# Kernel tuning notes

Measured on AMD Instinct MI355X. Metric: run time of the kernel, lower is better.

## Reference

```python
import jax, jax.numpy as jnp
import numpy as np

B, K_SLOTS, P = 4096, 8, 768
SLOT = P // 3          # 256, slot feature dim
HID = 256              # pres/up hidden width
NC, NP = 512, 512
LN_EPS = 1e-5


def _layernorm(x, g, b):
    m = jnp.mean(x, axis=-1, keepdims=True)
    v = jnp.var(x, axis=-1, keepdims=True)
    return (x - m) * jax.lax.rsqrt(v + LN_EPS) * g + b


def _mlp2(x, W1, b1, g, bt, W2, b2):
    # Linear -> LayerNorm -> ReLU -> Linear (torchvision ops.MLP with hidden=[256, out])
    h = jax.nn.relu(_layernorm(x @ W1 + b1, g, bt))
    return h @ W2 + b2


def setup_inputs() -> dict:
    key = jax.random.key(0)
    ks = jax.random.split(key, 24)
    rn = lambda k, shp, s=1.0: jax.random.normal(k, shp, dtype=jnp.float32) * s
    d = {
        "inst_embed": rn(ks[0], (B, P)),
        "slots": rn(ks[1], (B, K_SLOTS, SLOT)),
        # fc / fp: single Linear(p, p)
        "Wfc": rn(ks[2], (P, P), 1.0 / np.sqrt(P)),
        "bfc": jnp.zeros((P,), jnp.float32),
        "Wfp": rn(ks[3], (P, P), 1.0 / np.sqrt(P)),
        "bfp": jnp.zeros((P,), jnp.float32),
        # memory codebooks (plain randn per the original)
        "Kc": rn(ks[4], (NC, P)),
        "Vc": rn(ks[5], (NC, P)),
        "Kp": rn(ks[6], (NP, P)),
        "Vp": rn(ks[7], (NP, P)),
        # pres MLP: Linear(4p/3,256)+LN+ReLU, Linear(256,p/3)
        "pres_W1": rn(ks[8], (SLOT + P, HID), 1.0 / np.sqrt(SLOT + P)),
        "pres_b1": jnp.zeros((HID,), jnp.float32),
        "pres_g": jnp.ones((HID,), jnp.float32),
        "pres_bt": jnp.zeros((HID,), jnp.float32),
        "pres_W2": rn(ks[9], (HID, SLOT), 1.0 / np.sqrt(HID)),
        "pres_b2": jnp.zeros((SLOT,), jnp.float32),
        # up MLP: same shapes
        "up_W1": rn(ks[10], (SLOT + P, HID), 1.0 / np.sqrt(SLOT + P)),
        "up_b1": jnp.zeros((HID,), jnp.float32),
        "up_g": jnp.ones((HID,), jnp.float32),
        "up_bt": jnp.zeros((HID,), jnp.float32),
        "up_W2": rn(ks[11], (HID, SLOT), 1.0 / np.sqrt(HID)),
        "up_b2": jnp.zeros((SLOT,), jnp.float32),
    }
    return d


def reference(inst_embed, slots, Wfc, bfc, Wfp, bfp, Kc, Vc, Kp, Vp,
              pres_W1, pres_b1, pres_g, pres_bt, pres_W2, pres_b2,
              up_W1, up_b1, up_g, up_bt, up_W2, up_b2):
    scale = jnp.float32(np.sqrt(P))
    # selection: soft attention over the two codebooks
    Qc = inst_embed @ Wfc + bfc                     # [B, P]
    Qp = inst_embed @ Wfp + bfp                     # [B, P]
    c = jax.nn.softmax(jnp.einsum('bi,ci->bc', Qc, Kc) / scale, axis=-1) @ Vc  # [B, P]
    p = jax.nn.softmax(jnp.einsum('bi,pi->bp', Qp, Kp) / scale, axis=-1) @ Vp  # [B, P]
    # update: vectorized over the K slot loop of the original
    cb = jnp.broadcast_to(c[:, None, :], (B, K_SLOTS, P))
    pb = jnp.broadcast_to(p[:, None, :], (B, K_SLOTS, P))
    hc = jnp.concatenate([slots, cb], axis=-1)      # [B, K, SLOT+P]
    hp = jnp.concatenate([slots, pb], axis=-1)      # [B, K, SLOT+P]
    gate_pres = _mlp2(hc, pres_W1, pres_b1, pres_g, pres_bt, pres_W2, pres_b2)
    gate_up = _mlp2(hp, up_W1, up_b1, up_g, up_bt, up_W2, up_b2)
    return slots + gate_pres * gate_up              # [B, K, SLOT]
```

## Files before the change

kernel.cpp:

```cpp
#include <hip/hip_runtime.h>
#include <stdint.h>

#define BB    4096
#define KS    8
#define PP    768
#define SLOT  256
#define HID   256
#define NC    512
#define BKROWS (BB*KS)
typedef unsigned short u16;
typedef short bf16x8 __attribute__((ext_vector_type(8)));
typedef float f32x4  __attribute__((ext_vector_type(4)));

__device__ __forceinline__ u16 f2bf(float x) {
  union { float f; uint32_t u; } v; v.f = x;
  return (u16)((v.u + 0x7FFFu + ((v.u >> 16) & 1u)) >> 16);
}

__device__ __forceinline__ u16 f2h(float x) {
  union { _Float16 h; u16 u; } cv; cv.h = (_Float16)x; return cv.u;
}
__device__ __forceinline__ float h2f(u16 x) {
  union { u16 u; _Float16 h; } cv; cv.u = x; return (float)cv.h;
}

__device__ __forceinline__ void gload_lds16(u16* ldst, const u16* gsrc) {
  __builtin_amdgcn_global_load_lds(
      (const __attribute__((address_space(1))) void*)gsrc,
      (__attribute__((address_space(3))) void*)ldst, 16, 0, 0);
}

template<int EPI>
__device__ __forceinline__ void gemm_core64(
    const u16* __restrict__ A, int lda,
    const u16* __restrict__ B, int ldb,
    const float* __restrict__ bias,
    void* __restrict__ out, int ldo, int K,
    int blockRow, int blockCol, u16* lsA, u16* lsB)
{
  const int tid  = threadIdx.x;
  const int w    = tid >> 6;
  const int lane = tid & 63;
  const int wm   = w >> 1, wn = w & 1;
  const int rl   = lane >> 4, cl = lane & 15;

  f32x4 acc[2][4];
  const f32x4 zero = {0.f, 0.f, 0.f, 0.f};
#pragma unroll
  for (int i = 0; i < 2; ++i)
#pragma unroll
    for (int j = 0; j < 4; ++j) acc[i][j] = zero;

  const u16* Ablk = A + (size_t)blockRow * lda;
  const u16* Bblk = B + (size_t)blockCol * ldb;

  for (int k0 = 0; k0 < K; k0 += 64) {
#pragma unroll
    for (int i = 0; i < 2; ++i) {
      int seg   = i * 4 + w;
      int off16 = seg * 64 + lane;
      int row   = off16 >> 3;
      int chunk = (off16 & 7) ^ (row & 7);
      gload_lds16(lsA + seg * 512, Ablk + (size_t)row * lda + k0 + chunk * 8);
    }
#pragma unroll
    for (int i = 0; i < 4; ++i) {
      int seg   = i * 4 + w;
      int off16 = seg * 64 + lane;
      int row   = off16 >> 3;
      int chunk = (off16 & 7) ^ (row & 7);
      gload_lds16(lsB + seg * 512, Bblk + (size_t)row * ldb + k0 + chunk * 8);
    }
    __syncthreads();

#pragma unroll
    for (int ks = 0; ks < 2; ++ks) {
      bf16x8 aF[2], bF[4];
#pragma unroll
      for (int f = 0; f < 2; ++f) {
        int r  = wm * 32 + f * 16 + cl;
        int ca = ((ks * 4 + rl) ^ (r & 7)) * 8;
        aF[f] = *(const bf16x8*)(lsA + r * 64 + ca);
      }
#pragma unroll
      for (int f = 0; f < 4; ++f) {
        int rn = wn * 64 + f * 16 + cl;
        int cb = ((ks * 4 + rl) ^ (rn & 7)) * 8;
        bF[f] = *(const bf16x8*)(lsB + rn * 64 + cb);
      }
#pragma unroll
      for (int fm = 0; fm < 2; ++fm)
#pragma unroll
        for (int fn = 0; fn < 4; ++fn)
          acc[fm][fn] = __builtin_amdgcn_mfma_f32_16x16x32_bf16(
              aF[fm], bF[fn], acc[fm][fn], 0, 0, 0);
    }
    __syncthreads();
  }

#pragma unroll
  for (int fm = 0; fm < 2; ++fm) {
#pragma unroll
    for (int fn = 0; fn < 4; ++fn) {
      f32x4 v = acc[fm][fn];
#pragma unroll
      for (int r = 0; r < 4; ++r) {
        int grow = blockRow + wm * 32 + fm * 16 + rl * 4 + r;
        int gcol = blockCol + wn * 64 + fn * 16 + cl;
        float x = v[r];
        if constexpr (EPI == 2) {
          ((u16*)out)[(size_t)grow * ldo + gcol] = f2bf(x);
        } else if constexpr (EPI == 3) {
          x += bias[gcol];
          ((float*)out)[(size_t)grow * ldo + gcol] = x;
        } else if constexpr (EPI == 5) {
          x += bias[gcol];
          ((u16*)out)[(size_t)grow * ldo + gcol] = f2h(x);
        }
      }
    }
  }
}

template<int EPI>
__device__ __forceinline__ void gemm_core6464(
    const u16* __restrict__ A, int lda,
    const u16* __restrict__ B, int ldb,
    const float* __restrict__ bias,
    void* __restrict__ out, int ldo, int K,
    int blockRow, int blockCol, u16* lsA, u16* lsB)
{
  const int tid  = threadIdx.x;
  const int w    = tid >> 6;
  const int lane = tid & 63;
  const int wm   = w >> 1, wn = w & 1;
  const int rl   = lane >> 4, cl = lane & 15;

  f32x4 acc[2][2];
  const f32x4 zero = {0.f, 0.f, 0.f, 0.f};
#pragma unroll
  for (int i = 0; i < 2; ++i)
#pragma unroll
    for (int j = 0; j < 2; ++j) acc[i][j] = zero;

  const u16* Ablk = A + (size_t)blockRow * lda;
  const u16* Bblk = B + (size_t)blockCol * ldb;

  for (int k0 = 0; k0 < K; k0 += 64) {
#pragma unroll
    for (int i = 0; i < 2; ++i) {
      int seg   = i * 4 + w;
      int off16 = seg * 64 + lane;
      int row   = off16 >> 3;
      int chunk = (off16 & 7) ^ (row & 7);
      gload_lds16(lsA + seg * 512, Ablk + (size_t)row * lda + k0 + chunk * 8);
    }
#pragma unroll
    for (int i = 0; i < 2; ++i) {
      int seg   = i * 4 + w;
      int off16 = seg * 64 + lane;
      int row   = off16 >> 3;
      int chunk = (off16 & 7) ^ (row & 7);
      gload_lds16(lsB + seg * 512, Bblk + (size_t)row * ldb + k0 + chunk * 8);
    }
    __syncthreads();

#pragma unroll
    for (int ks = 0; ks < 2; ++ks) {
      bf16x8 aF[2], bF[2];
#pragma unroll
      for (int f = 0; f < 2; ++f) {
        int r  = wm * 32 + f * 16 + cl;
        int ca = ((ks * 4 + rl) ^ (r & 7)) * 8;
        aF[f] = *(const bf16x8*)(lsA + r * 64 + ca);
        int rn = wn * 32 + f * 16 + cl;
        int cb = ((ks * 4 + rl) ^ (rn & 7)) * 8;
        bF[f] = *(const bf16x8*)(lsB + rn * 64 + cb);
      }
#pragma unroll
      for (int fm = 0; fm < 2; ++fm)
#pragma unroll
        for (int fn = 0; fn < 2; ++fn)
          acc[fm][fn] = __builtin_amdgcn_mfma_f32_16x16x32_bf16(
              aF[fm], bF[fn], acc[fm][fn], 0, 0, 0);
    }
    __syncthreads();
  }

#pragma unroll
  for (int fm = 0; fm < 2; ++fm) {
#pragma unroll
    for (int fn = 0; fn < 2; ++fn) {
      f32x4 v = acc[fm][fn];
#pragma unroll
      for (int r = 0; r < 4; ++r) {
        int grow = blockRow + wm * 32 + fm * 16 + rl * 4 + r;
        int gcol = blockCol + wn * 32 + fn * 16 + cl;
        float x = v[r];
        if constexpr (EPI == 2) {
          ((u16*)out)[(size_t)grow * ldo + gcol] = f2bf(x);
        } else if constexpr (EPI == 3) {
          x += bias[gcol];
          ((float*)out)[(size_t)grow * ldo + gcol] = x;
        } else if constexpr (EPI == 5) {
          x += bias[gcol];
          ((u16*)out)[(size_t)grow * ldo + gcol] = f2h(x);
        }
      }
    }
  }
}

__device__ __forceinline__ void cvt_seg(const float* __restrict__ in,
                                        u16* __restrict__ outp, int b, int n4) {
  int i = b * 256 + threadIdx.x;
  if (i < n4) {
    float4 v = ((const float4*)in)[i];
    ushort4 o;
    o.x = f2bf(v.x); o.y = f2bf(v.y); o.z = f2bf(v.z); o.w = f2bf(v.w);
    ((ushort4*)outp)[i] = o;
  }
}

__device__ __forceinline__ void pack_seg(const float* __restrict__ s0,
                                         const float* __restrict__ s1,
                                         u16* __restrict__ dst, int b) {
  int br = b >> 4, ng = b & 15;
  const float* src = br ? s1 : s0;
  int w = threadIdx.x >> 6, lane = threadIdx.x & 63;
  int rl = lane >> 4, cl = lane & 15;
#pragma unroll
  for (int s = 0; s < 2; ++s) {
    int step = w * 2 + s;
    union { u16 u[8]; uint4 q; } o;
#pragma unroll
    for (int j = 0; j < 8; ++j)
      o.u[j] = f2bf(src[(size_t)(step * 32 + rl * 8 + j) * 256 + ng * 16 + cl]);
    *(uint4*)(dst + (size_t)(((br * 16 + ng) * 8 + step) * 64 + lane) * 8) = o.q;
  }
}

__global__ __launch_bounds__(256) void prep_all(
    const float* __restrict__ inst, const float* __restrict__ Kc,
    const float* __restrict__ Kp, const float* __restrict__ Wfc,
    const float* __restrict__ Wfp, const float* __restrict__ Vc,
    const float* __restrict__ Vp, const float* __restrict__ pW1,
    const float* __restrict__ uW1, const float* __restrict__ pW2,
    const float* __restrict__ uW2, const float* __restrict__ bfc,
    const float* __restrict__ bfp,
    u16* instb, u16* Kcb, u16* Kpb, u16* Wfcb, u16* Wfpb, u16* Vcb, u16* Vpb,
    u16* W1Tp, u16* W1Tu, u16* W1pk, u16* W2pk, float* sb)
{
  __shared__ float tile[32][33];
  int b = blockIdx.x;
  if (b < 3072)      { cvt_seg(inst, instb, b,        786432); return; }
  else if (b < 3456) { cvt_seg(Kc,   Kcb,   b - 3072,  98304); return; }
  else if (b < 3840) { cvt_seg(Kp,   Kpb,   b - 3456,  98304); return; }
  else if (b < 4416) { cvt_seg(Wfc,  Wfcb,  b - 3840, 147456); return; }
  else if (b < 4992) { cvt_seg(Wfp,  Wfpb,  b - 4416, 147456); return; }
  else if (b < 5376) { cvt_seg(Vc,   Vcb,   b - 4992,  98304); return; }
  else if (b < 5760) { cvt_seg(Vp,   Vpb,   b - 5376,  98304); return; }
  else if (b < 6272) {
    int bb = b - 5760;
    const float* in = (bb < 256) ? pW1 : uW1;
    u16* outp = (bb < 256) ? W1Tp : W1Tu;
    bb &= 255;
    int tc = (bb & 7) * 32, tr = (bb >> 3) * 32;
    int lx = threadIdx.x & 31, ly = threadIdx.x >> 5;
#pragma unroll
    for (int i = 0; i < 32; i += 8)
      tile[ly + i][lx] = in[(size_t)(tr + ly + i) * 256 + tc + lx];
    __syncthreads();
#pragma unroll
    for (int i = 0; i < 32; i += 8)
      outp[(size_t)(tc + ly + i) * 1024 + tr + lx] = f2bf(tile[lx][ly + i]);
    return;
  }
  else if (b < 6304) { pack_seg(pW1, uW1, W1pk, b - 6272); return; }
  else if (b < 6336) { pack_seg(pW2, uW2, W2pk, b - 6304); return; }
  else {
    int w = threadIdx.x >> 6, lane = threadIdx.x & 63;
    int row = (b - 6336) * 4 + w;
    int br = row >> 9, n = row & 511;
    const float* Kr = (br ? Kp : Kc) + (size_t)n * PP;
    const float* bf = br ? bfp : bfc;
    float s = 0.f;
#pragma unroll
    for (int j = 0; j < 12; ++j) s += Kr[lane + j * 64] * bf[lane + j * 64];
#pragma unroll
    for (int o = 32; o; o >>= 1) s += __shfl_xor(s, o);
    if (!lane) sb[row] = s;
  }
}

__global__ __launch_bounds__(256) void gemm_mixed(
    const u16* Kcb, const u16* Kpb, const u16* Wfcb, const u16* Wfpb,
    u16* KWc, u16* KWp,
    const u16* W1Tp, const u16* W1Tu, const u16* Vcb, const u16* Vpb,
    u16* VW1p, u16* VW1u)
{
  __shared__ u16 lsA[64 * 64];
  __shared__ u16 lsB[128 * 64];
  int b = blockIdx.x;
  if (b < 96) {
    int z = b / 48, r = b % 48;
    gemm_core64<2>(z ? Kpb : Kcb, PP, z ? Wfpb : Wfcb, PP, nullptr,
                   z ? KWp : KWc, PP, PP, (r & 7) * 64, (r >> 3) * 128, lsA, lsB);
  } else {
    int c = b - 96, z = c / 16, r = c % 16;
    gemm_core64<2>((z ? W1Tu : W1Tp) + 256, 1024, z ? Vpb : Vcb, PP, nullptr,
                   z ? VW1u : VW1p, NC, PP, (r & 3) * 64, (r >> 2) * 128, lsA, lsB);
  }
}

__global__ __launch_bounds__(256) void gemm_scores(
    const u16* instb, const u16* KW, const float* sb, u16* scH)
{
  __shared__ u16 lsA[64 * 64];
  __shared__ u16 lsB[64 * 64];
  gemm_core6464<5>(instb, PP, KW, PP, sb, scH, 1024, PP,
                   blockIdx.x * 64, blockIdx.y * 64, lsA, lsB);
}

__global__ __launch_bounds__(256) void gemm_t(
    const u16* Pb, const u16* VW1p, const u16* VW1u,
    const float* pb1, const float* ub1, float* t0, float* t1)
{
  __shared__ u16 lsA[64 * 64];
  __shared__ u16 lsB[64 * 64];
  int z = blockIdx.z;
  gemm_core6464<3>(Pb + (size_t)z * BB * NC, NC, z ? VW1u : VW1p, NC,
                   z ? ub1 : pb1, z ? t1 : t0, SLOT, NC,
                   blockIdx.x * 64, blockIdx.y * 64, lsA, lsB);
}

__global__ __launch_bounds__(256) void softmax_rows(const u16* __restrict__ scH,
                                                    u16* __restrict__ Pp) {
  int w = threadIdx.x >> 6, lane = threadIdx.x & 63;
  int row = blockIdx.x * 4 + w;
  int i = row >> 1, b = row & 1;
  const u16* src = scH + (size_t)i * 1024 + b * 512 + lane * 8;
  uint4 q = *(const uint4*)src;
  const u16* hp = (const u16*)&q;
  float vv[8];
#pragma unroll
  for (int j = 0; j < 8; ++j) vv[j] = h2f(hp[j]);
  float m = vv[0];
#pragma unroll
  for (int j = 1; j < 8; ++j) m = fmaxf(m, vv[j]);
#pragma unroll
  for (int o = 32; o; o >>= 1) m = fmaxf(m, __shfl_xor(m, o));
  const float alpha = 0.03608439182435161f;
  float e[8], s = 0.f;
#pragma unroll
  for (int j = 0; j < 8; ++j) { e[j] = __expf((vv[j] - m) * alpha); s += e[j]; }
#pragma unroll
  for (int o = 32; o; o >>= 1) s += __shfl_xor(s, o);
  float inv = 1.f / s;
  union { u16 u[8]; uint4 q; } ou;
#pragma unroll
  for (int j = 0; j < 8; ++j) ou.u[j] = f2bf(e[j] * inv);
  *(uint4*)(Pp + ((size_t)b * BB + i) * 512 + lane * 8) = ou.q;
}

__global__ __launch_bounds__(512, 4) void fused_update(
    const float* __restrict__ slots,
    const float* __restrict__ t0, const float* __restrict__ t1,
    const u16* __restrict__ W1pk, const u16* __restrict__ W2pk,
    const float* __restrict__ pg, const float* __restrict__ pbt,
    const float* __restrict__ ug, const float* __restrict__ ubt,
    const float* __restrict__ pb2, const float* __restrict__ ub2,
    float* __restrict__ outp)
{
  __shared__ u16 lsH[2][32 * 256];
  __shared__ float lstat[2][32][16];
  __shared__ float lfin[2][32][2];

  const int tid = threadIdx.x, w = tid >> 6, lane = tid & 63;
  const int rl = lane >> 4, cl = lane & 15;
  const int blockRow = blockIdx.x * 32;

  u16* lsA = lsH[0];

#pragma unroll
  for (int it = 0; it < 4; ++it) {
    int L = it * 512 + tid;
    int row = L >> 6, qc = L & 63;
    float4 v = *(const float4*)(slots + (size_t)(blockRow + row) * 256 + qc * 4);
    ushort4 b; b.x = f2bf(v.x); b.y = f2bf(v.y); b.z = f2bf(v.z); b.w = f2bf(v.w);
    int chunk = qc >> 1, half = qc & 1;
    *(ushort4*)(lsA + row * 256 + (((chunk ^ (row & 7)) << 3) + half * 4)) = b;
  }
  __syncthreads();

  f32x4 acc[2][4];
  const f32x4 zero = {0.f, 0.f, 0.f, 0.f};
#pragma unroll
  for (int i = 0; i < 2; ++i)
#pragma unroll
    for (int j = 0; j < 4; ++j) acc[i][j] = zero;

#define MF(A, B, C) C = __builtin_amdgcn_mfma_f32_16x16x32_bf16(A, B, C, 0, 0, 0);

  {
    bf16x8 pb[3][2], ub[3][2];
#define FR1(NG, S) (*(const bf16x8*)(W1pk + (size_t)(((NG) * 8 + (S)) * 64 + lane) * 8))
#define LDW1(SL, S) { pb[SL][0] = FR1(w * 2, S);      pb[SL][1] = FR1(w * 2 + 1, S);  \
                      ub[SL][0] = FR1(16 + w * 2, S); ub[SL][1] = FR1(17 + w * 2, S); \
                      asm volatile("" ::: "memory"); }
    LDW1(0, 0) LDW1(1, 1) LDW1(2, 2)
#pragma unroll
    for (int s = 0; s < 8; ++s) {
      const int sl = s % 3;
      bf16x8 a0 = *(const bf16x8*)(lsA + cl * 256 + (((s * 4 + rl) ^ (cl & 7)) << 3));
      bf16x8 a1 = *(const bf16x8*)(lsA + (16 + cl) * 256 + (((s * 4 + rl) ^ (cl & 7)) << 3));
      MF(a0, pb[sl][0], acc[0][0]) MF(a1, pb[sl][0], acc[1][0])
      MF(a0, pb[sl][1], acc[0][1]) MF(a1, pb[sl][1], acc[1][1])
      MF(a0, ub[sl][0], acc[0][2]) MF(a1, ub[sl][0], acc[1][2])
      MF(a0, ub[sl][1], acc[0][3]) MF(a1, ub[sl][1], acc[1][3])
      if (s < 5) LDW1(sl, s + 3)
    }
#undef LDW1
#undef FR1
  }

#pragma unroll
  for (int fm = 0; fm < 2; ++fm) {
    size_t trr = (size_t)(blockIdx.x * 4 + fm * 2 + (rl >> 1)) * 256;
#pragma unroll
    for (int fn = 0; fn < 2; ++fn) {
      int col = w * 32 + fn * 16 + cl;
      float tp = t0[trr + col], tu = t1[trr + col];
#pragma unroll
      for (int r = 0; r < 4; ++r) {
        acc[fm][fn][r]     += tp;
        acc[fm][2 + fn][r] += tu;
      }
    }
  }

#pragma unroll
  for (int fm = 0; fm < 2; ++fm)
#pragma unroll
    for (int br = 0; br < 2; ++br) {
      f32x4 s = acc[fm][br * 2] + acc[fm][br * 2 + 1];
      f32x4 q = acc[fm][br * 2] * acc[fm][br * 2] + acc[fm][br * 2 + 1] * acc[fm][br * 2 + 1];
#pragma unroll
      for (int o = 1; o < 16; o <<= 1) {
#pragma unroll
        for (int r = 0; r < 4; ++r) {
          s[r] += __shfl_xor(s[r], o);
          q[r] += __shfl_xor(q[r], o);
        }
      }
      if (cl == 0) {
#pragma unroll
        for (int r = 0; r < 4; ++r) {
          int row = fm * 16 + rl * 4 + r;
          lstat[br][row][w]     = s[r];
          lstat[br][row][8 + w] = q[r];
        }
      }
    }
  __syncthreads();

  if (tid < 64) {
    int fb = tid >> 5, row = tid & 31;
    f32x4 a = *(const f32x4*)&lstat[fb][row][0];
    f32x4 b = *(const f32x4*)&lstat[fb][row][4];
    f32x4 c = *(const f32x4*)&lstat[fb][row][8];
    f32x4 d = *(const f32x4*)&lstat[fb][row][12];
    float ss = a[0] + a[1] + a[2] + a[3] + b[0] + b[1] + b[2] + b[3];
    float qq = c[0] + c[1] + c[2] + c[3] + d[0] + d[1] + d[2] + d[3];
    float mu = ss * (1.f / 256.f);
    lfin[fb][row][0] = mu;
    lfin[fb][row][1] = rsqrtf(qq * (1.f / 256.f) - mu * mu + 1e-5f);
  }
  __syncthreads();

  {
    float gv[2][2], btv[2][2];
#pragma unroll
    for (int fn = 0; fn < 2; ++fn) {
      int col = w * 32 + fn * 16 + cl;
      gv[0][fn] = pg[col];  btv[0][fn] = pbt[col];
      gv[1][fn] = ug[col];  btv[1][fn] = ubt[col];
    }
#pragma unroll
    for (int fm = 0; fm < 2; ++fm) {
      float mean[2][4], rstd[2][4];
#pragma unroll
      for (int r = 0; r < 4; ++r) {
        int row = fm * 16 + rl * 4 + r;
        mean[0][r] = lfin[0][row][0]; rstd[0][r] = lfin[0][row][1];
        mean[1][r] = lfin[1][row][0]; rstd[1][r] = lfin[1][row][1];
      }
#pragma unroll
      for (int br = 0; br < 2; ++br)
#pragma unroll
        for (int fn = 0; fn < 2; ++fn) {
          int col = w * 32 + fn * 16 + cl;
#pragma unroll
          for (int r = 0; r < 4; ++r) {
            int row = fm * 16 + rl * 4 + r;
            float h = fmaxf((acc[fm][br * 2 + fn][r] - mean[br][r]) * rstd[br][r]
                            * gv[br][fn] + btv[br][fn], 0.f);
            lsH[br][row * 256 + (((col >> 3) ^ (row & 7)) << 3) + (col & 7)] = f2bf(h);
          }
        }
    }
  }
#pragma unroll
  for (int i = 0; i < 2; ++i)
#pragma unroll
    for (int j = 0; j < 4; ++j) acc[i][j] = zero;
  __syncthreads();

  const int brw = w >> 2, wc = w & 3;
  const u16* hsrc = lsH[brw];
  const float* b2src = brw ? ub2 : pb2;
  float b2v[4];
#pragma unroll
  for (int fn = 0; fn < 4; ++fn) b2v[fn] = b2src[wc * 64 + fn * 16 + cl];

  {
    bf16x8 bq[3][4];
#define FR2(NG, S) (*(const bf16x8*)(W2pk + (size_t)(((NG) * 8 + (S)) * 64 + lane) * 8))
#define LDW2(SL, S) { bq[SL][0] = FR2(brw * 16 + wc * 4,     S); \
                      bq[SL][1] = FR2(brw * 16 + wc * 4 + 1, S); \
                      bq[SL][2] = FR2(brw * 16 + wc * 4 + 2, S); \
                      bq[SL][3] = FR2(brw * 16 + wc * 4 + 3, S); \
                      asm volatile("" ::: "memory"); }
    LDW2(0, 0) LDW2(1, 1) LDW2(2, 2)
#pragma unroll
    for (int s = 0; s < 8; ++s) {
      const int sl = s % 3;
      bf16x8 a0 = *(const bf16x8*)(hsrc + cl * 256 + (((s * 4 + rl) ^ (cl & 7)) << 3));
      bf16x8 a1 = *(const bf16x8*)(hsrc + (16 + cl) * 256 + (((s * 4 + rl) ^ (cl & 7)) << 3));
      MF(a0, bq[sl][0], acc[0][0]) MF(a1, bq[sl][0], acc[1][0])
      MF(a0, bq[sl][1], acc[0][1]) MF(a1, bq[sl][1], acc[1][1])
      MF(a0, bq[sl][2], acc[0][2]) MF(a1, bq[sl][2], acc[1][2])
      MF(a0, bq[sl][3], acc[0][3]) MF(a1, bq[sl][3], acc[1][3])
      if (s < 5) LDW2(sl, s + 3)
    }
#undef LDW2
#undef FR2
  }
#undef MF
  __syncthreads();

  float* xbuf = (float*)&lsH[0][0];
  const int base = wc * 2048;
  if (brw == 0) {
#pragma unroll
    for (int fm = 0; fm < 2; ++fm)
#pragma unroll
      for (int fn = 0; fn < 4; ++fn)
#pragma unroll
        for (int r = 0; r < 4; ++r)
          xbuf[base + ((fm * 4 + fn) * 4 + r) * 64 + lane] = acc[fm][fn][r] + b2v[fn];
  }
  __syncthreads();

  if (brw == 1) {
#pragma unroll
    for (int fm = 0; fm < 2; ++fm)
#pragma unroll
      for (int fn = 0; fn < 4; ++fn)
#pragma unroll
        for (int r = 0; r < 4; ++r) {
          float gp = xbuf[base + ((fm * 4 + fn) * 4 + r) * 64 + lane];
          float gu = acc[fm][fn][r] + b2v[fn];
          int row = blockRow + fm * 16 + rl * 4 + r;
          int col = wc * 64 + fn * 16 + cl;
          size_t idx = (size_t)row * 256 + col;
          outp[idx] = slots[idx] + gp * gu;
        }
  }
}

extern "C" void kernel_launch(void* const* d_in, const int* in_sizes, int n_in,
                              void* d_out, int out_size, void* d_ws, size_t ws_size,
                              hipStream_t stream) {
  const float* inst  = (const float*)d_in[0];
  const float* slots = (const float*)d_in[1];
  const float* Wfc   = (const float*)d_in[2];
  const float* bfc   = (const float*)d_in[3];
  const float* Wfp   = (const float*)d_in[4];
  const float* bfp   = (const float*)d_in[5];
  const float* Kc    = (const float*)d_in[6];
  const float* Vc    = (const float*)d_in[7];
  const float* Kp    = (const float*)d_in[8];
  const float* Vp    = (const float*)d_in[9];
  const float* pW1   = (const float*)d_in[10];
  const float* pb1   = (const float*)d_in[11];
  const float* pg    = (const float*)d_in[12];
  const float* pbt   = (const float*)d_in[13];
  const float* pW2   = (const float*)d_in[14];
  const float* pb2   = (const float*)d_in[15];
  const float* uW1   = (const float*)d_in[16];
  const float* ub1   = (const float*)d_in[17];
  const float* ug    = (const float*)d_in[18];
  const float* ubt   = (const float*)d_in[19];
  const float* uW2   = (const float*)d_in[20];
  const float* ub2   = (const float*)d_in[21];
  float* out = (float*)d_out;
  char*  ws  = (char*)d_ws;

  const size_t OFF_INST  = 0;
  const size_t OFF_KC    = OFF_INST  + 6291456;
  const size_t OFF_KP    = OFF_KC    + 786432;
  const size_t OFF_WFCB  = OFF_KP    + 786432;
  const size_t OFF_WFPB  = OFF_WFCB  + 1179648;
  const size_t OFF_VCB   = OFF_WFPB  + 1179648;
  const size_t OFF_VPB   = OFF_VCB   + 786432;
  const size_t OFF_W1TP  = OFF_VPB   + 786432;
  const size_t OFF_W1TU  = OFF_W1TP  + 524288;
  const size_t OFF_W1PK  = OFF_W1TU  + 524288;
  const size_t OFF_W2PK  = OFF_W1PK  + 262144;
  const size_t OFF_KW    = OFF_W2PK  + 262144;
  const size_t OFF_VW1   = OFF_KW    + 1572864;
  const size_t OFF_SB    = OFF_VW1   + 524288;
  const size_t OFF_T     = OFF_SB    + 4096;
  const size_t OFF_SC    = OFF_T     + 8388608;
  const size_t OFF_P     = OFF_SC    + 8388608;

  u16*   instb = (u16*)(ws + OFF_INST);
  u16*   Kcb   = (u16*)(ws + OFF_KC);
  u16*   Kpb   = (u16*)(ws + OFF_KP);
  u16*   Wfcb  = (u16*)(ws + OFF_WFCB);
  u16*   Wfpb  = (u16*)(ws + OFF_WFPB);
  u16*   Vcb   = (u16*)(ws + OFF_VCB);
  u16*   Vpb   = (u16*)(ws + OFF_VPB);
  u16*   W1Tp  = (u16*)(ws + OFF_W1TP);
  u16*   W1Tu  = (u16*)(ws + OFF_W1TU);
  u16*   W1pk  = (u16*)(ws + OFF_W1PK);
  u16*   W2pk  = (u16*)(ws + OFF_W2PK);
  u16*   KWc   = (u16*)(ws + OFF_KW);
  u16*   KWp   = KWc + (size_t)NC * PP;
  u16*   VW1p  = (u16*)(ws + OFF_VW1);
  u16*   VW1u  = VW1p + (size_t)SLOT * NC;
  float* sb    = (float*)(ws + OFF_SB);
  float* t0    = (float*)(ws + OFF_T);
  float* t1    = t0 + (size_t)BB * SLOT;
  u16*   scH   = (u16*)(ws + OFF_SC);
  u16*   Pb    = (u16*)(ws + OFF_P);

  prep_all<<<dim3(6592), 256, 0, stream>>>(
      inst, Kc, Kp, Wfc, Wfp, Vc, Vp, pW1, uW1, pW2, uW2, bfc, bfp,
      instb, Kcb, Kpb, Wfcb, Wfpb, Vcb, Vpb, W1Tp, W1Tu, W1pk, W2pk, sb);

  gemm_mixed<<<dim3(128), 256, 0, stream>>>(
      Kcb, Kpb, Wfcb, Wfpb, KWc, KWp, W1Tp, W1Tu, Vcb, Vpb, VW1p, VW1u);

  gemm_scores<<<dim3(64, 16), 256, 0, stream>>>(instb, KWc, sb, scH);

  softmax_rows<<<dim3(2048), 256, 0, stream>>>(scH, Pb);

  gemm_t<<<dim3(64, 4, 2), 256, 0, stream>>>(Pb, VW1p, VW1u, pb1, ub1, t0, t1);

  fused_update<<<dim3(1024), 512, 0, stream>>>(
      slots, t0, t1, W1pk, W2pk, pg, pbt, ug, ubt, pb2, ub2, out);

  (void)in_sizes; (void)n_in; (void)out_size; (void)ws_size;
}
```

Baseline: 87.02 us.

## Fuse inst bf16 conversion into scores GEMM and retile precompute GEMMs

Removes the separate fp32->bf16 conversion pass over inst_embed from prep_all. The scores GEMM now loads fp32 inst rows directly, converts them in registers and writes swizzled bf16 into LDS, which avoids one write and one re-read of a 6 MB buffer. The mixed precompute GEMM switches to 64x64 tiles, doubling its block count to 256 for better CU coverage. The fused update kernel now issues the t0/t1 and W2 fragment loads earlier to overlap their latency with other work. In exchange, the scores kernel's A-tile load becomes a synchronous register path instead of an async LDS load, and each scores block repeats the conversion.

```diff
diff --git a/kernel.cpp b/kernel.cpp
--- a/kernel.cpp
+++ b/kernel.cpp
@@ -28,98 +28,6 @@
   __builtin_amdgcn_global_load_lds(
       (const __attribute__((address_space(1))) void*)gsrc,
       (__attribute__((address_space(3))) void*)ldst, 16, 0, 0);
-}
-
-template<int EPI>
-__device__ __forceinline__ void gemm_core64(
-    const u16* __restrict__ A, int lda,
-    const u16* __restrict__ B, int ldb,
-    const float* __restrict__ bias,
-    void* __restrict__ out, int ldo, int K,
-    int blockRow, int blockCol, u16* lsA, u16* lsB)
-{
-  const int tid  = threadIdx.x;
-  const int w    = tid >> 6;
-  const int lane = tid & 63;
-  const int wm   = w >> 1, wn = w & 1;
-  const int rl   = lane >> 4, cl = lane & 15;
-
-  f32x4 acc[2][4];
-  const f32x4 zero = {0.f, 0.f, 0.f, 0.f};
-#pragma unroll
-  for (int i = 0; i < 2; ++i)
-#pragma unroll
-    for (int j = 0; j < 4; ++j) acc[i][j] = zero;
-
-  const u16* Ablk = A + (size_t)blockRow * lda;
-  const u16* Bblk = B + (size_t)blockCol * ldb;
-
-  for (int k0 = 0; k0 < K; k0 += 64) {
-#pragma unroll
-    for (int i = 0; i < 2; ++i) {
-      int seg   = i * 4 + w;
-      int off16 = seg * 64 + lane;
-      int row   = off16 >> 3;
-      int chunk = (off16 & 7) ^ (row & 7);
-      gload_lds16(lsA + seg * 512, Ablk + (size_t)row * lda + k0 + chunk * 8);
-    }
-#pragma unroll
-    for (int i = 0; i < 4; ++i) {
-      int seg   = i * 4 + w;
-      int off16 = seg * 64 + lane;
-      int row   = off16 >> 3;
-      int chunk = (off16 & 7) ^ (row & 7);
-      gload_lds16(lsB + seg * 512, Bblk + (size_t)row * ldb + k0 + chunk * 8);
-    }
-    __syncthreads();
-
-#pragma unroll
-    for (int ks = 0; ks < 2; ++ks) {
-      bf16x8 aF[2], bF[4];
-#pragma unroll
-      for (int f = 0; f < 2; ++f) {
-        int r  = wm * 32 + f * 16 + cl;
-        int ca = ((ks * 4 + rl) ^ (r & 7)) * 8;
-        aF[f] = *(const bf16x8*)(lsA + r * 64 + ca);
-      }
-#pragma unroll
-      for (int f = 0; f < 4; ++f) {
-        int rn = wn * 64 + f * 16 + cl;
-        int cb = ((ks * 4 + rl) ^ (rn & 7)) * 8;
-        bF[f] = *(const bf16x8*)(lsB + rn * 64 + cb);
-      }
-#pragma unroll
-      for (int fm = 0; fm < 2; ++fm)
-#pragma unroll
-        for (int fn = 0; fn < 4; ++fn)
-          acc[fm][fn] = __builtin_amdgcn_mfma_f32_16x16x32_bf16(
-              aF[fm], bF[fn], acc[fm][fn], 0, 0, 0);
-    }
-    __syncthreads();
-  }
-
-#pragma unroll
-  for (int fm = 0; fm < 2; ++fm) {
-#pragma unroll
-    for (int fn = 0; fn < 4; ++fn) {
-      f32x4 v = acc[fm][fn];
-#pragma unroll
-      for (int r = 0; r < 4; ++r) {
-        int grow = blockRow + wm * 32 + fm * 16 + rl * 4 + r;
-        int gcol = blockCol + wn * 64 + fn * 16 + cl;
-        float x = v[r];
-        if constexpr (EPI == 2) {
-          ((u16*)out)[(size_t)grow * ldo + gcol] = f2bf(x);
-        } else if constexpr (EPI == 3) {
-          x += bias[gcol];
-          ((float*)out)[(size_t)grow * ldo + gcol] = x;
-        } else if constexpr (EPI == 5) {
-          x += bias[gcol];
-          ((u16*)out)[(size_t)grow * ldo + gcol] = f2h(x);
-        }
-      }
-    }
-  }
 }
 
 template<int EPI>
@@ -241,27 +149,25 @@
 }
 
 __global__ __launch_bounds__(256) void prep_all(
-    const float* __restrict__ inst, const float* __restrict__ Kc,
-    const float* __restrict__ Kp, const float* __restrict__ Wfc,
-    const float* __restrict__ Wfp, const float* __restrict__ Vc,
-    const float* __restrict__ Vp, const float* __restrict__ pW1,
-    const float* __restrict__ uW1, const float* __restrict__ pW2,
-    const float* __restrict__ uW2, const float* __restrict__ bfc,
-    const float* __restrict__ bfp,
-    u16* instb, u16* Kcb, u16* Kpb, u16* Wfcb, u16* Wfpb, u16* Vcb, u16* Vpb,
+    const float* __restrict__ Kc, const float* __restrict__ Kp,
+    const float* __restrict__ Wfc, const float* __restrict__ Wfp,
+    const float* __restrict__ Vc, const float* __restrict__ Vp,
+    const float* __restrict__ pW1, const float* __restrict__ uW1,
+    const float* __restrict__ pW2, const float* __restrict__ uW2,
+    const float* __restrict__ bfc, const float* __restrict__ bfp,
+    u16* Kcb, u16* Kpb, u16* Wfcb, u16* Wfpb, u16* Vcb, u16* Vpb,
     u16* W1Tp, u16* W1Tu, u16* W1pk, u16* W2pk, float* sb)
 {
   __shared__ float tile[32][33];
   int b = blockIdx.x;
-  if (b < 3072)      { cvt_seg(inst, instb, b,        786432); return; }
-  else if (b < 3456) { cvt_seg(Kc,   Kcb,   b - 3072,  98304); return; }
-  else if (b < 3840) { cvt_seg(Kp,   Kpb,   b - 3456,  98304); return; }
-  else if (b < 4416) { cvt_seg(Wfc,  Wfcb,  b - 3840, 147456); return; }
-  else if (b < 4992) { cvt_seg(Wfp,  Wfpb,  b - 4416, 147456); return; }
-  else if (b < 5376) { cvt_seg(Vc,   Vcb,   b - 4992,  98304); return; }
-  else if (b < 5760) { cvt_seg(Vp,   Vpb,   b - 5376,  98304); return; }
-  else if (b < 6272) {
-    int bb = b - 5760;
+  if (b < 384)       { cvt_seg(Kc,   Kcb,   b,         98304); return; }
+  else if (b < 768)  { cvt_seg(Kp,   Kpb,   b - 384,   98304); return; }
+  else if (b < 1344) { cvt_seg(Wfc,  Wfcb,  b - 768,  147456); return; }
+  else if (b < 1920) { cvt_seg(Wfp,  Wfpb,  b - 1344, 147456); return; }
+  else if (b < 2304) { cvt_seg(Vc,   Vcb,   b - 1920,  98304); return; }
+  else if (b < 2688) { cvt_seg(Vp,   Vpb,   b - 2304,  98304); return; }
+  else if (b < 3200) {
+    int bb = b - 2688;
     const float* in = (bb < 256) ? pW1 : uW1;
     u16* outp = (bb < 256) ? W1Tp : W1Tu;
     bb &= 255;
@@ -276,11 +182,11 @@
       outp[(size_t)(tc + ly + i) * 1024 + tr + lx] = f2bf(tile[lx][ly + i]);
     return;
   }
-  else if (b < 6304) { pack_seg(pW1, uW1, W1pk, b - 6272); return; }
-  else if (b < 6336) { pack_seg(pW2, uW2, W2pk, b - 6304); return; }
+  else if (b < 3232) { pack_seg(pW1, uW1, W1pk, b - 3200); return; }
+  else if (b < 3264) { pack_seg(pW2, uW2, W2pk, b - 3232); return; }
   else {
     int w = threadIdx.x >> 6, lane = threadIdx.x & 63;
-    int row = (b - 6336) * 4 + w;
+    int row = (b - 3264) * 4 + w;
     int br = row >> 9, n = row & 511;
     const float* Kr = (br ? Kp : Kc) + (size_t)n * PP;
     const float* bf = br ? bfp : bfc;
@@ -300,26 +206,103 @@
     u16* VW1p, u16* VW1u)
 {
   __shared__ u16 lsA[64 * 64];
-  __shared__ u16 lsB[128 * 64];
+  __shared__ u16 lsB[64 * 64];
   int b = blockIdx.x;
-  if (b < 96) {
-    int z = b / 48, r = b % 48;
-    gemm_core64<2>(z ? Kpb : Kcb, PP, z ? Wfpb : Wfcb, PP, nullptr,
-                   z ? KWp : KWc, PP, PP, (r & 7) * 64, (r >> 3) * 128, lsA, lsB);
+  if (b < 192) {
+    int z = b / 96, r = b % 96;
+    gemm_core6464<2>(z ? Kpb : Kcb, PP, z ? Wfpb : Wfcb, PP, nullptr,
+                     z ? KWp : KWc, PP, PP, (r & 7) * 64, (r >> 3) * 64, lsA, lsB);
   } else {
-    int c = b - 96, z = c / 16, r = c % 16;
-    gemm_core64<2>((z ? W1Tu : W1Tp) + 256, 1024, z ? Vpb : Vcb, PP, nullptr,
-                   z ? VW1u : VW1p, NC, PP, (r & 3) * 64, (r >> 2) * 128, lsA, lsB);
+    int c = b - 192, z = c / 32, r = c % 32;
+    gemm_core6464<2>((z ? W1Tu : W1Tp) + 256, 1024, z ? Vpb : Vcb, PP, nullptr,
+                     z ? VW1u : VW1p, NC, PP, (r & 3) * 64, (r >> 2) * 64, lsA, lsB);
   }
 }
 
 __global__ __launch_bounds__(256) void gemm_scores(
-    const u16* instb, const u16* KW, const float* sb, u16* scH)
+    const float* __restrict__ inst, const u16* __restrict__ KW,
+    const float* __restrict__ sb, u16* __restrict__ scH)
 {
   __shared__ u16 lsA[64 * 64];
   __shared__ u16 lsB[64 * 64];
-  gemm_core6464<5>(instb, PP, KW, PP, sb, scH, 1024, PP,
-                   blockIdx.x * 64, blockIdx.y * 64, lsA, lsB);
+  const int tid  = threadIdx.x;
+  const int w    = tid >> 6;
+  const int lane = tid & 63;
+  const int wm   = w >> 1, wn = w & 1;
+  const int rl   = lane >> 4, cl = lane & 15;
+  const int blockRow = blockIdx.x * 64;
+  const int blockCol = blockIdx.y * 64;
+
+  const int arow = tid >> 2;
+  const int kseg = (tid & 3) * 16;
+
+  f32x4 acc[2][2];
+  const f32x4 zero = {0.f, 0.f, 0.f, 0.f};
+#pragma unroll
+  for (int i = 0; i < 2; ++i)
+#pragma unroll
+    for (int j = 0; j < 2; ++j) acc[i][j] = zero;
+
+  const float* Asrc = inst + (size_t)(blockRow + arow) * PP + kseg;
+  const u16*   Bblk = KW + (size_t)blockCol * PP;
+
+  for (int k0 = 0; k0 < PP; k0 += 64) {
+    union { u16 u[8]; uint4 q; } c0, c1;
+#pragma unroll
+    for (int j = 0; j < 2; ++j) {
+      float4 v0 = *(const float4*)(Asrc + k0 + j * 8);
+      float4 v1 = *(const float4*)(Asrc + k0 + j * 8 + 4);
+      u16* dd = j ? c1.u : c0.u;
+      dd[0] = f2bf(v0.x); dd[1] = f2bf(v0.y); dd[2] = f2bf(v0.z); dd[3] = f2bf(v0.w);
+      dd[4] = f2bf(v1.x); dd[5] = f2bf(v1.y); dd[6] = f2bf(v1.z); dd[7] = f2bf(v1.w);
+    }
+    int cc = kseg >> 3;
+    *(uint4*)(lsA + arow * 64 + (((cc     ) ^ (arow & 7)) << 3)) = c0.q;
+    *(uint4*)(lsA + arow * 64 + (((cc + 1) ^ (arow & 7)) << 3)) = c1.q;
+#pragma unroll
+    for (int i = 0; i < 2; ++i) {
+      int seg   = i * 4 + w;
+      int off16 = seg * 64 + lane;
+      int row   = off16 >> 3;
+      int chunk = (off16 & 7) ^ (row & 7);
+      gload_lds16(lsB + seg * 512, Bblk + (size_t)row * PP + k0 + chunk * 8);
+    }
+    __syncthreads();
+
+#pragma unroll
+    for (int ks = 0; ks < 2; ++ks) {
+      bf16x8 aF[2], bF[2];
+#pragma unroll
+      for (int f = 0; f < 2; ++f) {
+        int r  = wm * 32 + f * 16 + cl;
+        int ca = ((ks * 4 + rl) ^ (r & 7)) * 8;
+        aF[f] = *(const bf16x8*)(lsA + r * 64 + ca);
+        int rn = wn * 32 + f * 16 + cl;
+        int cb = ((ks * 4 + rl) ^ (rn & 7)) * 8;
+        bF[f] = *(const bf16x8*)(lsB + rn * 64 + cb);
+      }
+#pragma unroll
+      for (int fm = 0; fm < 2; ++fm)
+#pragma unroll
+        for (int fn = 0; fn < 2; ++fn)
+          acc[fm][fn] = __builtin_amdgcn_mfma_f32_16x16x32_bf16(
+              aF[fm], bF[fn], acc[fm][fn], 0, 0, 0);
+    }
+    __syncthreads();
+  }
+
+#pragma unroll
+  for (int fm = 0; fm < 2; ++fm)
+#pragma unroll
+    for (int fn = 0; fn < 2; ++fn) {
+      f32x4 v = acc[fm][fn];
+#pragma unroll
+      for (int r = 0; r < 4; ++r) {
+        int grow = blockRow + wm * 32 + fm * 16 + rl * 4 + r;
+        int gcol = blockCol + wn * 32 + fn * 16 + cl;
+        scH[(size_t)grow * 1024 + gcol] = f2h(v[r] + sb[gcol]);
+      }
+    }
 }
 
 __global__ __launch_bounds__(256) void gemm_t(
@@ -391,53 +374,59 @@
     int chunk = qc >> 1, half = qc & 1;
     *(ushort4*)(lsA + row * 256 + (((chunk ^ (row & 7)) << 3) + half * 4)) = b;
   }
-  __syncthreads();
-
-  f32x4 acc[2][4];
-  const f32x4 zero = {0.f, 0.f, 0.f, 0.f};
-#pragma unroll
-  for (int i = 0; i < 2; ++i)
-#pragma unroll
-    for (int j = 0; j < 4; ++j) acc[i][j] = zero;
+
+  float tp_[2][2], tu_[2][2];
+#pragma unroll
+  for (int fm = 0; fm < 2; ++fm) {
+    size_t trr = (size_t)(blockIdx.x * 4 + fm * 2 + (rl >> 1)) * 256;
+#pragma unroll
+    for (int fn = 0; fn < 2; ++fn) {
+      int col = w * 32 + fn * 16 + cl;
+      tp_[fm][fn] = t0[trr + col];
+      tu_[fm][fn] = t1[trr + col];
+    }
+  }
 
 #define MF(A, B, C) C = __builtin_amdgcn_mfma_f32_16x16x32_bf16(A, B, C, 0, 0, 0);
 
-  {
-    bf16x8 pb[3][2], ub[3][2];
+  bf16x8 pb[3][2], ub[3][2];
 #define FR1(NG, S) (*(const bf16x8*)(W1pk + (size_t)(((NG) * 8 + (S)) * 64 + lane) * 8))
 #define LDW1(SL, S) { pb[SL][0] = FR1(w * 2, S);      pb[SL][1] = FR1(w * 2 + 1, S);  \
                       ub[SL][0] = FR1(16 + w * 2, S); ub[SL][1] = FR1(17 + w * 2, S); \
                       asm volatile("" ::: "memory"); }
-    LDW1(0, 0) LDW1(1, 1) LDW1(2, 2)
-#pragma unroll
-    for (int s = 0; s < 8; ++s) {
-      const int sl = s % 3;
-      bf16x8 a0 = *(const bf16x8*)(lsA + cl * 256 + (((s * 4 + rl) ^ (cl & 7)) << 3));
-      bf16x8 a1 = *(const bf16x8*)(lsA + (16 + cl) * 256 + (((s * 4 + rl) ^ (cl & 7)) << 3));
-      MF(a0, pb[sl][0], acc[0][0]) MF(a1, pb[sl][0], acc[1][0])
-      MF(a0, pb[sl][1], acc[0][1]) MF(a1, pb[sl][1], acc[1][1])
-      MF(a0, ub[sl][0], acc[0][2]) MF(a1, ub[sl][0], acc[1][2])
-      MF(a0, ub[sl][1], acc[0][3]) MF(a1, ub[sl][1], acc[1][3])
-      if (s < 5) LDW1(sl, s + 3)
-    }
+  LDW1(0, 0) LDW1(1, 1) LDW1(2, 2)
+  __syncthreads();
+
+  f32x4 acc[2][4];
+  const f32x4 zero = {0.f, 0.f, 0.f, 0.f};
+#pragma unroll
+  for (int i = 0; i < 2; ++i)
+#pragma unroll
+    for (int j = 0; j < 4; ++j) acc[i][j] = zero;
+
+#pragma unroll
+  for (int s = 0; s < 8; ++s) {
+    const int sl = s % 3;
+    bf16x8 a0 = *(const bf16x8*)(lsA + cl * 256 + (((s * 4 + rl) ^ (cl & 7)) << 3));
+    bf16x8 a1 = *(const bf16x8*)(lsA + (16 + cl) * 256 + (((s * 4 + rl) ^ (cl & 7)) << 3));
+    MF(a0, pb[sl][0], acc[0][0]) MF(a1, pb[sl][0], acc[1][0])
+    MF(a0, pb[sl][1], acc[0][1]) MF(a1, pb[sl][1], acc[1][1])
+    MF(a0, ub[sl][0], acc[0][2]) MF(a1, ub[sl][0], acc[1][2])
+    MF(a0, ub[sl][1], acc[0][3]) MF(a1, ub[sl][1], acc[1][3])
+    if (s < 5) LDW1(sl, s + 3)
+  }
 #undef LDW1
 #undef FR1
-  }
-
-#pragma unroll
-  for (int fm = 0; fm < 2; ++fm) {
-    size_t trr = (size_t)(blockIdx.x * 4 + fm * 2 + (rl >> 1)) * 256;
-#pragma unroll
-    for (int fn = 0; fn < 2; ++fn) {
-      int col = w * 32 + fn * 16 + cl;
-      float tp = t0[trr + col], tu = t1[trr + col];
+
+#pragma unroll
+  for (int fm = 0; fm < 2; ++fm)
+#pragma unroll
+    for (int fn = 0; fn < 2; ++fn)
 #pragma unroll
       for (int r = 0; r < 4; ++r) {
-        acc[fm][fn][r]     += tp;
-        acc[fm][2 + fn][r] += tu;
-      }
-    }
-  }
+        acc[fm][fn][r]     += tp_[fm][fn];
+        acc[fm][2 + fn][r] += tu_[fm][fn];
+      }
 
 #pragma unroll
   for (int fm = 0; fm < 2; ++fm)
@@ -478,6 +467,22 @@
   }
   __syncthreads();
 
+  const int brw = w >> 2, wc = w & 3;
+  const u16* hsrc = lsH[brw];
+  const float* b2src = brw ? ub2 : pb2;
+  float b2v[4];
+#pragma unroll
+  for (int fn = 0; fn < 4; ++fn) b2v[fn] = b2src[wc * 64 + fn * 16 + cl];
+
+  bf16x8 bq[3][4];
+#define FR2(NG, S) (*(const bf16x8*)(W2pk + (size_t)(((NG) * 8 + (S)) * 64 + lane) * 8))
+#define LDW2(SL, S) { bq[SL][0] = FR2(brw * 16 + wc * 4,     S); \
+                      bq[SL][1] = FR2(brw * 16 + wc * 4 + 1, S); \
+                      bq[SL][2] = FR2(brw * 16 + wc * 4 + 2, S); \
+                      bq[SL][3] = FR2(brw * 16 + wc * 4 + 3, S); \
+                      asm volatile("" ::: "memory"); }
+  LDW2(0, 0)
+
   {
     float gv[2][2], btv[2][2];
 #pragma unroll
@@ -516,36 +521,20 @@
     for (int j = 0; j < 4; ++j) acc[i][j] = zero;
   __syncthreads();
 
-  const int brw = w >> 2, wc = w & 3;
-  const u16* hsrc = lsH[brw];
-  const float* b2src = brw ? ub2 : pb2;
-  float b2v[4];
-#pragma unroll
-  for (int fn = 0; fn < 4; ++fn) b2v[fn] = b2src[wc * 64 + fn * 16 + cl];
-
-  {
-    bf16x8 bq[3][4];
-#define FR2(NG, S) (*(const bf16x8*)(W2pk + (size_t)(((NG) * 8 + (S)) * 64 + lane) * 8))
-#define LDW2(SL, S) { bq[SL][0] = FR2(brw * 16 + wc * 4,     S); \
-                      bq[SL][1] = FR2(brw * 16 + wc * 4 + 1, S); \
-                      bq[SL][2] = FR2(brw * 16 + wc * 4 + 2, S); \
-                      bq[SL][3] = FR2(brw * 16 + wc * 4 + 3, S); \
-                      asm volatile("" ::: "memory"); }
-    LDW2(0, 0) LDW2(1, 1) LDW2(2, 2)
-#pragma unroll
-    for (int s = 0; s < 8; ++s) {
-      const int sl = s % 3;
-      bf16x8 a0 = *(const bf16x8*)(hsrc + cl * 256 + (((s * 4 + rl) ^ (cl & 7)) << 3));
-      bf16x8 a1 = *(const bf16x8*)(hsrc + (16 + cl) * 256 + (((s * 4 + rl) ^ (cl & 7)) << 3));
-      MF(a0, bq[sl][0], acc[0][0]) MF(a1, bq[sl][0], acc[1][0])
-      MF(a0, bq[sl][1], acc[0][1]) MF(a1, bq[sl][1], acc[1][1])
-      MF(a0, bq[sl][2], acc[0][2]) MF(a1, bq[sl][2], acc[1][2])
-      MF(a0, bq[sl][3], acc[0][3]) MF(a1, bq[sl][3], acc[1][3])
-      if (s < 5) LDW2(sl, s + 3)
-    }
+  LDW2(1, 1) LDW2(2, 2)
+#pragma unroll
+  for (int s = 0; s < 8; ++s) {
+    const int sl = s % 3;
+    bf16x8 a0 = *(const bf16x8*)(hsrc + cl * 256 + (((s * 4 + rl) ^ (cl & 7)) << 3));
+    bf16x8 a1 = *(const bf16x8*)(hsrc + (16 + cl) * 256 + (((s * 4 + rl) ^ (cl & 7)) << 3));
+    MF(a0, bq[sl][0], acc[0][0]) MF(a1, bq[sl][0], acc[1][0])
+    MF(a0, bq[sl][1], acc[0][1]) MF(a1, bq[sl][1], acc[1][1])
+    MF(a0, bq[sl][2], acc[0][2]) MF(a1, bq[sl][2], acc[1][2])
+    MF(a0, bq[sl][3], acc[0][3]) MF(a1, bq[sl][3], acc[1][3])
+    if (s < 5) LDW2(sl, s + 3)
+  }
 #undef LDW2
 #undef FR2
-  }
 #undef MF
   __syncthreads();
 
@@ -607,8 +596,7 @@
   float* out = (float*)d_out;
   char*  ws  = (char*)d_ws;
 
-  const size_t OFF_INST  = 0;
-  const size_t OFF_KC    = OFF_INST  + 6291456;
+  const size_t OFF_KC    = 0;
   const size_t OFF_KP    = OFF_KC    + 786432;
   const size_t OFF_WFCB  = OFF_KP    + 786432;
   const size_t OFF_WFPB  = OFF_WFCB  + 1179648;
@@ -625,7 +613,6 @@
   const size_t OFF_SC    = OFF_T     + 8388608;
   const size_t OFF_P     = OFF_SC    + 8388608;
 
-  u16*   instb = (u16*)(ws + OFF_INST);
   u16*   Kcb   = (u16*)(ws + OFF_KC);
   u16*   Kpb   = (u16*)(ws + OFF_KP);
   u16*   Wfcb  = (u16*)(ws + OFF_WFCB);
@@ -646,14 +633,14 @@
   u16*   scH   = (u16*)(ws + OFF_SC);
   u16*   Pb    = (u16*)(ws + OFF_P);
 
-  prep_all<<<dim3(6592), 256, 0, stream>>>(
-      inst, Kc, Kp, Wfc, Wfp, Vc, Vp, pW1, uW1, pW2, uW2, bfc, bfp,
-      instb, Kcb, Kpb, Wfcb, Wfpb, Vcb, Vpb, W1Tp, W1Tu, W1pk, W2pk, sb);
-
-  gemm_mixed<<<dim3(128), 256, 0, stream>>>(
+  prep_all<<<dim3(3520), 256, 0, stream>>>(
+      Kc, Kp, Wfc, Wfp, Vc, Vp, pW1, uW1, pW2, uW2, bfc, bfp,
+      Kcb, Kpb, Wfcb, Wfpb, Vcb, Vpb, W1Tp, W1Tu, W1pk, W2pk, sb);
+
+  gemm_mixed<<<dim3(256), 256, 0, stream>>>(
       Kcb, Kpb, Wfcb, Wfpb, KWc, KWp, W1Tp, W1Tu, Vcb, Vpb, VW1p, VW1u);
 
-  gemm_scores<<<dim3(64, 16), 256, 0, stream>>>(instb, KWc, sb, scH);
+  gemm_scores<<<dim3(64, 16), 256, 0, stream>>>(inst, KWc, sb, scH);
 
   softmax_rows<<<dim3(2048), 256, 0, stream>>>(scH, Pb);
 
```

Measured after the change: 90.50 us. 4.0% more time.
